# Kernel optimization log

Measured on AMD Instinct MI355X. Metric: run time of the kernel, lower is better.

## Reference

```python
import jax, jax.numpy as jnp
import numpy as np

NUM_HEADS = 16
ROPE_BASE = 10000.0


def apply_rope(x):
    # x: [B, T, H, D]; torchtune-style interleaved-pair RoPE, positions 0..T-1
    B, T, H, D = x.shape
    inv_freq = 1.0 / (ROPE_BASE ** (jnp.arange(0, D, 2, dtype=jnp.float32) / D))  # [D/2]
    pos = jnp.arange(T, dtype=jnp.float32)
    freqs = pos[:, None] * inv_freq[None, :]              # [T, D/2]
    cos = jnp.cos(freqs)[None, :, None, :].astype(x.dtype)
    sin = jnp.sin(freqs)[None, :, None, :].astype(x.dtype)
    x1 = x[..., 0::2]
    x2 = x[..., 1::2]
    o1 = x1 * cos - x2 * sin
    o2 = x2 * cos + x1 * sin
    return jnp.stack([o1, o2], axis=-1).reshape(B, T, H, D)


def setup_inputs() -> dict:
    key = jax.random.key(0)
    k1, k2, k3 = jax.random.split(key, 3)
    B, T, C = 2, 8192, 1024
    x = jax.random.normal(k1, (B, T, C), dtype=jnp.float32)
    # torch Linear weight layout [out_features, in_features]; fan-in scaling
    Wqkv = jax.random.normal(k2, (3 * C, C), dtype=jnp.float32) * (C ** -0.5)
    Wout = jax.random.normal(k3, (C, C), dtype=jnp.float32) * (C ** -0.5)
    return {"x": x, "Wqkv": Wqkv, "Wout": Wout}


def reference(x, Wqkv, Wout):
    B, T, C = x.shape
    H = NUM_HEADS
    D = C // H
    qkv = (x @ Wqkv.T).reshape(B, T, 3, H, D)
    q, k, v = qkv[:, :, 0], qkv[:, :, 1], qkv[:, :, 2]   # each [B, T, H, D]
    q = apply_rope(q)
    k = apply_rope(k)
    # Faithful to source: SDPA is called on [B, T, H, D] WITHOUT transposing,
    # so torch attends over the heads axis (L = H) with (B, T) as batch dims.
    scale = 1.0 / jnp.sqrt(jnp.asarray(D, dtype=x.dtype))
    scores = jnp.einsum('btqd,btkd->btqk', q, k) * scale  # [B, T, H, H]
    attn = jax.nn.softmax(scores, axis=-1)
    out = jnp.einsum('btqk,btkd->btqd', attn, v)          # [B, T, H, D]
    # Replicate attn_output.transpose(1, 2).contiguous().view(B, T, C)
    out = out.transpose(0, 2, 1, 3).reshape(B, T, C)
    return out @ Wout.T
```

## Files before the change

### kernel.cpp

```cpp
#include <hip/hip_runtime.h>
#include <stdint.h>

#define TT 8192
#define BT 16384
#define MCH 8192

typedef __attribute__((ext_vector_type(8))) __bf16 bf16x8;
typedef __attribute__((ext_vector_type(4))) __bf16 bf16x4;
typedef __attribute__((ext_vector_type(4))) short short4v;
typedef __attribute__((ext_vector_type(4))) float floatx4;

__device__ __forceinline__ float bf2f(unsigned short h) {
  union { unsigned u; float f; } x; x.u = ((unsigned)h) << 16; return x.f;
}
__device__ __forceinline__ unsigned short f2bf(float f) {
  union { float f; unsigned u; } x; x.f = f;
  unsigned r = (x.u + 0x7fffu + ((x.u >> 16) & 1u)) >> 16;
  return (unsigned short)r;
}
__device__ __forceinline__ void async16(const void* g, void* l) {
  __builtin_amdgcn_global_load_lds(
      (__attribute__((address_space(1))) void*)g,
      (__attribute__((address_space(3))) void*)l, 16, 0, 0);
}

__global__ __launch_bounds__(256) void cvt_f2b(
    const float* __restrict__ src, unsigned short* __restrict__ dst, int n4) {
  const int i = blockIdx.x * 256 + threadIdx.x;
  if (i < n4) {
    const float4 f = ((const float4*)src)[i];
    union { uint2 u2; unsigned short s[4]; } o;
    o.s[0] = f2bf(f.x); o.s[1] = f2bf(f.y);
    o.s[2] = f2bf(f.z); o.s[3] = f2bf(f.w);
    ((uint2*)dst)[i] = o.u2;
  }
}

__global__ __launch_bounds__(256) void prep_k(
    const float* __restrict__ Wqkv, const float* __restrict__ Wout,
    unsigned short* __restrict__ Wqkvb, unsigned short* __restrict__ Woutb,
    float2* __restrict__ tab) {
  const int bx = blockIdx.x;
  const int tid = threadIdx.x;
  if (bx < 1024) {
    const int i = bx * 256 + tid;
    const int t = i >> 5, p = i & 31;
    const float f = (float)t * exp2f((float)p * -0.41524101186092f);
    float s, c;
    sincosf(f, &s, &c);
    tab[i] = make_float2(c, s);
  } else {
    const float* src;
    unsigned short* dst;
    int i;
    if (bx < 4096) { src = Wqkv; dst = Wqkvb; i = (bx - 1024) * 256 + tid; }
    else           { src = Wout; dst = Woutb; i = (bx - 4096) * 256 + tid; }
    const float4 f = ((const float4*)src)[i];
    union { uint2 u2; unsigned short s[4]; } o;
    o.s[0] = f2bf(f.x); o.s[1] = f2bf(f.y);
    o.s[2] = f2bf(f.z); o.s[3] = f2bf(f.w);
    ((uint2*)dst)[i] = o.u2;
  }
}

template <bool CF32>
__global__ __launch_bounds__(512, 4) void gemm_k32(
    const unsigned short* __restrict__ A,
    const unsigned short* __restrict__ W,
    void* __restrict__ C,
    int M, int N, int K)
{
  __shared__ __align__(16) unsigned short sm[2][(256 + 128) * 32];

  const int tid  = threadIdx.x;
  const int lane = tid & 63;
  const int wid  = tid >> 6;
  const int wr   = wid >> 1;
  const int wc   = wid & 1;
  const int lm   = lane & 15;
  const int kg   = lane >> 4;
  const int cxor = (lm >> 1) & 3;

  const int nb  = N >> 7;
  const int cpx = (int)gridDim.x >> 3;
  const int bid = blockIdx.x;
  const int swz = (bid & 7) * cpx + (bid >> 3);
  const int bm  = swz / nb;
  const int bn  = swz % nb;

  const int NT = K >> 5;

  const int sr  = lane >> 2;
  const int scb = lane & 3;
  const unsigned short* gsrc0;
  const unsigned short* gsrc1;
  const unsigned short* gsrc2;
  {
    const int r0 = wid * 16 + sr;
    const int r1 = 128 + r0;
    const int rB = wid * 16 + sr;
    gsrc0 = A + (size_t)(bm * 256 + r0) * (size_t)K + ((scb ^ ((r0 >> 1) & 3)) << 3);
    gsrc1 = A + (size_t)(bm * 256 + r1) * (size_t)K + ((scb ^ ((r1 >> 1) & 3)) << 3);
    gsrc2 = W + (size_t)(bn * 128 + rB) * (size_t)K + ((scb ^ ((rB >> 1) & 3)) << 3);
  }
  const int ld0 = wid * 1024;
  const int ld1 = 8192 + wid * 1024;
  const int ld2 = 16384 + wid * 1024;

  auto stage_tile = [&](int tt) {
    char* lb = (char*)sm[tt & 1];
    const size_t koff = (size_t)tt << 5;
    async16(gsrc0 + koff, lb + ld0);
    async16(gsrc1 + koff, lb + ld1);
    async16(gsrc2 + koff, lb + ld2);
  };

  floatx4 acc[4][4];
  floatx4 z = {0.f, 0.f, 0.f, 0.f};
#pragma unroll
  for (int i = 0; i < 4; ++i)
#pragma unroll
    for (int j = 0; j < 4; ++j) acc[i][j] = z;

  stage_tile(0);
  stage_tile(1);
  asm volatile("s_waitcnt vmcnt(3)" ::: "memory");
  __builtin_amdgcn_s_barrier();
  __builtin_amdgcn_sched_barrier(0);

  for (int t = 0; t < NT; ++t) {
    const unsigned short* Ab = sm[t & 1];
    const unsigned short* Bb = Ab + 256 * 32;

    bf16x8 af[4], bfr[4];
#pragma unroll
    for (int i = 0; i < 4; ++i) {
      const int rr = wr * 64 + i * 16 + lm;
      af[i] = *(const bf16x8*)(Ab + rr * 32 + ((kg ^ cxor) << 3));
    }
#pragma unroll
    for (int j = 0; j < 4; ++j) {
      const int rr = wc * 64 + j * 16 + lm;
      bfr[j] = *(const bf16x8*)(Bb + rr * 32 + ((kg ^ cxor) << 3));
    }

    __builtin_amdgcn_s_barrier();
    asm volatile("s_waitcnt lgkmcnt(0)" ::: "memory");
    __builtin_amdgcn_sched_barrier(0);

    if (t + 2 < NT) stage_tile(t + 2);

    __builtin_amdgcn_s_setprio(1);
#pragma unroll
    for (int i = 0; i < 4; ++i)
#pragma unroll
      for (int j = 0; j < 4; ++j)
        acc[i][j] = __builtin_amdgcn_mfma_f32_16x16x32_bf16(
            af[i], bfr[j], acc[i][j], 0, 0, 0);
    __builtin_amdgcn_s_setprio(0);

    if (t + 1 < NT) {
      if (t + 2 < NT)
        asm volatile("s_waitcnt vmcnt(3)" ::: "memory");
      else
        asm volatile("s_waitcnt vmcnt(0)" ::: "memory");
      __builtin_amdgcn_s_barrier();
      __builtin_amdgcn_sched_barrier(0);
    }
  }

#pragma unroll
  for (int i = 0; i < 4; ++i) {
    const int row0 = bm * 256 + wr * 64 + i * 16 + kg * 4;
#pragma unroll
    for (int j = 0; j < 4; ++j) {
      const int col = bn * 128 + wc * 64 + j * 16 + lm;
#pragma unroll
      for (int r = 0; r < 4; ++r) {
        if (CF32)
          ((float*)C)[(size_t)(row0 + r) * N + col] = acc[i][j][r];
        else
          ((unsigned short*)C)[(size_t)(row0 + r) * N + col] = f2bf(acc[i][j][r]);
      }
    }
  }
}

#if defined(__has_builtin)
#if __has_builtin(__builtin_amdgcn_mfma_f32_16x16x16_bf16)
#define PV_MFMA 1
#define PV_MFMA_CALL(a, b, c) __builtin_amdgcn_mfma_f32_16x16x16_bf16( \
    *(bf16x4*)&(a), *(bf16x4*)&(b), (c), 0, 0, 0)
#elif __has_builtin(__builtin_amdgcn_mfma_f32_16x16x16bf16_1k)
#define PV_MFMA 1
#define PV_MFMA_CALL(a, b, c) __builtin_amdgcn_mfma_f32_16x16x16bf16_1k( \
    (a), (b), (c), 0, 0, 0)
#else
#define PV_MFMA 0
#endif
#else
#define PV_MFMA 0
#endif

__global__ __launch_bounds__(256, 4) void attn_rope_k(
    const unsigned short* __restrict__ qkv,
    const float2* __restrict__ tab,
    unsigned short* __restrict__ Y,
    int base)
{
  __shared__ __align__(16) unsigned short sV[4][16 * 72];
#if !PV_MFMA
  __shared__ float sP[4][256];
#endif

  const int wave = threadIdx.x >> 6;
  const int lane = threadIdx.x & 63;
  const int lm   = lane & 15;
  const int quad = lane >> 4;
  const int ml0  = blockIdx.x * 8 + wave * 2;
  unsigned short* VB = sV[wave];

  const int hlo = lane >> 3;
  const int d0  = (lane & 7) * 8;
  const int p0  = d0 >> 1;

  uint4 R[2][6];
  float4 CS[2][2];
  int tA[2], bA[2];
#pragma unroll
  for (int tk = 0; tk < 2; ++tk) {
    const int m = base + ml0 + tk;
    tA[tk] = m & (TT - 1);
    bA[tk] = m >> 13;
    const uint4* row = (const uint4*)(qkv + (size_t)(ml0 + tk) * 3072);
#pragma unroll
    for (int i = 0; i < 6; ++i) R[tk][i] = row[lane + 64 * i];
    CS[tk][0] = *(const float4*)(tab + (tA[tk] << 5) + p0);
    CS[tk][1] = *(const float4*)(tab + (tA[tk] << 5) + p0 + 2);
  }

#pragma unroll
  for (int tk = 0; tk < 2; ++tk) {
    const int t = tA[tk];
    const float cs[4] = {CS[tk][0].x, CS[tk][0].z, CS[tk][1].x, CS[tk][1].z};
    const float sn[4] = {CS[tk][0].y, CS[tk][0].w, CS[tk][1].y, CS[tk][1].w};

    uint4 P[4];
#pragma unroll
    for (int i = 0; i < 4; ++i) {
      union { uint4 u4; unsigned short s[8]; } cv;
      cv.u4 = R[tk][i];
      float f[8];
#pragma unroll
      for (int j = 0; j < 8; ++j) f[j] = bf2f(cv.s[j]);
#pragma unroll
      for (int j = 0; j < 4; ++j) {
        const float x1 = f[2 * j], x2 = f[2 * j + 1];
        cv.s[2 * j]     = f2bf(x1 * cs[j] - x2 * sn[j]);
        cv.s[2 * j + 1] = f2bf(x2 * cs[j] + x1 * sn[j]);
      }
      P[i] = cv.u4;
    }

    *(uint4*)(VB + hlo * 72 + d0)       = R[tk][4];
    *(uint4*)(VB + (8 + hlo) * 72 + d0) = R[tk][5];

    __builtin_amdgcn_s_setprio(1);
    floatx4 accS = {0.f, 0.f, 0.f, 0.f};
#pragma unroll
    for (int half = 0; half < 2; ++half) {
      const int bpi = (((lm & 7) * 8) + half * 4 + quad) * 4;
      union { int w[4]; bf16x8 v; } kf, qf;
#pragma unroll
      for (int w = 0; w < 4; ++w) {
        const int q0 = __builtin_amdgcn_ds_bpermute(bpi, (int)(&P[0].x)[w]);
        const int q1 = __builtin_amdgcn_ds_bpermute(bpi, (int)(&P[1].x)[w]);
        qf.w[w] = lm < 8 ? q0 : q1;
        const int k0 = __builtin_amdgcn_ds_bpermute(bpi, (int)(&P[2].x)[w]);
        const int k1 = __builtin_amdgcn_ds_bpermute(bpi, (int)(&P[3].x)[w]);
        kf.w[w] = lm < 8 ? k0 : k1;
      }
      accS = __builtin_amdgcn_mfma_f32_16x16x32_bf16(kf.v, qf.v, accS, 0, 0, 0);
    }

    float s4[4];
    float mx = -1e30f;
#pragma unroll
    for (int j = 0; j < 4; ++j) { s4[j] = accS[j] * 0.125f; mx = fmaxf(mx, s4[j]); }
    mx = fmaxf(mx, __shfl_xor(mx, 16, 64));
    mx = fmaxf(mx, __shfl_xor(mx, 32, 64));
    float sum = 0.f;
#pragma unroll
    for (int j = 0; j < 4; ++j) { s4[j] = __expf(s4[j] - mx); sum += s4[j]; }
    sum += __shfl_xor(sum, 16, 64);
    sum += __shfl_xor(sum, 32, 64);
    const float inv = 1.0f / sum;

#if PV_MFMA
    union { short4v v; unsigned short s[4]; } pf;
#pragma unroll
    for (int j = 0; j < 4; ++j) pf.s[j] = f2bf(s4[j] * inv);
    unsigned short vs[16];
#pragma unroll
    for (int dtile = 0; dtile < 4; ++dtile)
#pragma unroll
      for (int j = 0; j < 4; ++j)
        vs[dtile * 4 + j] = VB[(quad * 4 + j) * 72 + dtile * 16 + lm];
#pragma unroll
    for (int dtile = 0; dtile < 4; ++dtile) {
      union { short4v v; unsigned short s[4]; } vf;
#pragma unroll
      for (int j = 0; j < 4; ++j) vf.s[j] = vs[dtile * 4 + j];
      floatx4 accO = {0.f, 0.f, 0.f, 0.f};
      accO = PV_MFMA_CALL(pf.v, vf.v, accO);
      const int col = (t & 15) * 64 + dtile * 16 + lm;
#pragma unroll
      for (int r = 0; r < 4; ++r) {
        const size_t rr = (size_t)bA[tk] * TT + (size_t)(quad * 4 + r) * 512 + (t >> 4);
        Y[rr * 1024 + col] = f2bf(accO[r]);
      }
    }
    __builtin_amdgcn_s_setprio(0);
#else
    __builtin_amdgcn_s_setprio(0);
    float* Pp = sP[wave];
#pragma unroll
    for (int j = 0; j < 4; ++j) Pp[(quad * 4 + j) * 16 + lm] = s4[j] * inv;
    asm volatile("s_waitcnt lgkmcnt(0)" ::: "memory");
    __builtin_amdgcn_sched_barrier(0);
    float o[16];
#pragma unroll
    for (int dd = 0; dd < 16; ++dd) o[dd] = 0.f;
#pragma unroll
    for (int kh = 0; kh < 16; ++kh) {
      const float a = Pp[kh * 16 + lm];
      union { uint4 u4; unsigned short s[8]; } v0, v1;
      v0.u4 = *(const uint4*)(VB + kh * 72 + quad * 16);
      v1.u4 = *(const uint4*)(VB + kh * 72 + quad * 16 + 8);
#pragma unroll
      for (int dd = 0; dd < 8; ++dd) {
        o[dd]     += a * bf2f(v0.s[dd]);
        o[dd + 8] += a * bf2f(v1.s[dd]);
      }
    }
    const size_t rr = (size_t)bA[tk] * TT + (size_t)lm * 512 + (t >> 4);
    unsigned short* yp = Y + rr * 1024 + (t & 15) * 64 + quad * 16;
    union { uint4 u4; unsigned short s[8]; } o1, o2;
#pragma unroll
    for (int dd = 0; dd < 8; ++dd) o1.s[dd] = f2bf(o[dd]);
#pragma unroll
    for (int dd = 0; dd < 8; ++dd) o2.s[dd] = f2bf(o[8 + dd]);
    ((uint4*)yp)[0] = o1.u4;
    ((uint4*)yp)[1] = o2.u4;
#endif
  }
}

extern "C" void kernel_launch(void* const* d_in, const int* in_sizes, int n_in,
                              void* d_out, int out_size, void* d_ws, size_t ws_size,
                              hipStream_t stream) {
  const float* x    = (const float*)d_in[0];
  const float* Wqkv = (const float*)d_in[1];
  const float* Wout = (const float*)d_in[2];
  float* out = (float*)d_out;

  unsigned short* Y     = (unsigned short*)d_ws;
  unsigned short* Wqkvb = Y + (size_t)BT * 1024;
  unsigned short* Woutb = Wqkvb + (size_t)3072 * 1024;
  unsigned short* xb    = Woutb + (size_t)1024 * 1024;
  unsigned short* qkvC  = (unsigned short*)d_out;
  float2* tab           = (float2*)((char*)d_out + (size_t)52 * 1024 * 1024);

  prep_k<<<dim3(5120), dim3(256), 0, stream>>>(Wqkv, Wout, Wqkvb, Woutb, tab);

  for (int base = 0; base < BT; base += MCH) {
    cvt_f2b<<<dim3(MCH * 1024 / 4 / 256), dim3(256), 0, stream>>>(
        x + (size_t)base * 1024, xb, MCH * 1024 / 4);
    gemm_k32<false><<<dim3((MCH / 256) * (3072 / 128)), dim3(512), 0, stream>>>(
        xb, Wqkvb, qkvC, MCH, 3072, 1024);
    attn_rope_k<<<dim3(MCH / 8), dim3(256), 0, stream>>>(qkvC, tab, Y, base);
  }

  gemm_k32<true><<<dim3((BT / 256) * (1024 / 128)), dim3(512), 0, stream>>>(
      Y, Woutb, out, BT, 1024, 1024);
}
```

Baseline: 312.5 us.

## Stage attention output in LDS for coalesced 16-byte stores, one token per wave

```diff
diff --git a/kernel.cpp b/kernel.cpp
--- a/kernel.cpp
+++ b/kernel.cpp
@@ -209,6 +209,7 @@
     int base)
 {
   __shared__ __align__(16) unsigned short sV[4][16 * 72];
+  __shared__ __align__(16) unsigned short sO[4][1024];
 #if !PV_MFMA
   __shared__ float sP[4][256];
 #endif
@@ -217,142 +218,139 @@
   const int lane = threadIdx.x & 63;
   const int lm   = lane & 15;
   const int quad = lane >> 4;
-  const int ml0  = blockIdx.x * 8 + wave * 2;
+  const int ml   = blockIdx.x * 4 + wave;
+  const int m    = base + ml;
+  const int t    = m & (TT - 1);
   unsigned short* VB = sV[wave];
 
   const int hlo = lane >> 3;
   const int d0  = (lane & 7) * 8;
   const int p0  = d0 >> 1;
 
-  uint4 R[2][6];
-  float4 CS[2][2];
-  int tA[2], bA[2];
-#pragma unroll
-  for (int tk = 0; tk < 2; ++tk) {
-    const int m = base + ml0 + tk;
-    tA[tk] = m & (TT - 1);
-    bA[tk] = m >> 13;
-    const uint4* row = (const uint4*)(qkv + (size_t)(ml0 + tk) * 3072);
-#pragma unroll
-    for (int i = 0; i < 6; ++i) R[tk][i] = row[lane + 64 * i];
-    CS[tk][0] = *(const float4*)(tab + (tA[tk] << 5) + p0);
-    CS[tk][1] = *(const float4*)(tab + (tA[tk] << 5) + p0 + 2);
-  }
-
-#pragma unroll
-  for (int tk = 0; tk < 2; ++tk) {
-    const int t = tA[tk];
-    const float cs[4] = {CS[tk][0].x, CS[tk][0].z, CS[tk][1].x, CS[tk][1].z};
-    const float sn[4] = {CS[tk][0].y, CS[tk][0].w, CS[tk][1].y, CS[tk][1].w};
-
-    uint4 P[4];
-#pragma unroll
-    for (int i = 0; i < 4; ++i) {
-      union { uint4 u4; unsigned short s[8]; } cv;
-      cv.u4 = R[tk][i];
-      float f[8];
-#pragma unroll
-      for (int j = 0; j < 8; ++j) f[j] = bf2f(cv.s[j]);
-#pragma unroll
-      for (int j = 0; j < 4; ++j) {
-        const float x1 = f[2 * j], x2 = f[2 * j + 1];
-        cv.s[2 * j]     = f2bf(x1 * cs[j] - x2 * sn[j]);
-        cv.s[2 * j + 1] = f2bf(x2 * cs[j] + x1 * sn[j]);
-      }
-      P[i] = cv.u4;
-    }
-
-    *(uint4*)(VB + hlo * 72 + d0)       = R[tk][4];
-    *(uint4*)(VB + (8 + hlo) * 72 + d0) = R[tk][5];
-
-    __builtin_amdgcn_s_setprio(1);
-    floatx4 accS = {0.f, 0.f, 0.f, 0.f};
-#pragma unroll
-    for (int half = 0; half < 2; ++half) {
-      const int bpi = (((lm & 7) * 8) + half * 4 + quad) * 4;
-      union { int w[4]; bf16x8 v; } kf, qf;
-#pragma unroll
-      for (int w = 0; w < 4; ++w) {
-        const int q0 = __builtin_amdgcn_ds_bpermute(bpi, (int)(&P[0].x)[w]);
-        const int q1 = __builtin_amdgcn_ds_bpermute(bpi, (int)(&P[1].x)[w]);
-        qf.w[w] = lm < 8 ? q0 : q1;
-        const int k0 = __builtin_amdgcn_ds_bpermute(bpi, (int)(&P[2].x)[w]);
-        const int k1 = __builtin_amdgcn_ds_bpermute(bpi, (int)(&P[3].x)[w]);
-        kf.w[w] = lm < 8 ? k0 : k1;
-      }
-      accS = __builtin_amdgcn_mfma_f32_16x16x32_bf16(kf.v, qf.v, accS, 0, 0, 0);
-    }
-
-    float s4[4];
-    float mx = -1e30f;
-#pragma unroll
-    for (int j = 0; j < 4; ++j) { s4[j] = accS[j] * 0.125f; mx = fmaxf(mx, s4[j]); }
-    mx = fmaxf(mx, __shfl_xor(mx, 16, 64));
-    mx = fmaxf(mx, __shfl_xor(mx, 32, 64));
-    float sum = 0.f;
-#pragma unroll
-    for (int j = 0; j < 4; ++j) { s4[j] = __expf(s4[j] - mx); sum += s4[j]; }
-    sum += __shfl_xor(sum, 16, 64);
-    sum += __shfl_xor(sum, 32, 64);
-    const float inv = 1.0f / sum;
+  uint4 R[6];
+  const uint4* row = (const uint4*)(qkv + (size_t)ml * 3072);
+#pragma unroll
+  for (int i = 0; i < 6; ++i) R[i] = row[lane + 64 * i];
+  const float4 CS0 = *(const float4*)(tab + (t << 5) + p0);
+  const float4 CS1 = *(const float4*)(tab + (t << 5) + p0 + 2);
+  const float cs[4] = {CS0.x, CS0.z, CS1.x, CS1.z};
+  const float sn[4] = {CS0.y, CS0.w, CS1.y, CS1.w};
+
+  uint4 P[4];
+#pragma unroll
+  for (int i = 0; i < 4; ++i) {
+    union { uint4 u4; unsigned short s[8]; } cv;
+    cv.u4 = R[i];
+    float f[8];
+#pragma unroll
+    for (int j = 0; j < 8; ++j) f[j] = bf2f(cv.s[j]);
+#pragma unroll
+    for (int j = 0; j < 4; ++j) {
+      const float x1 = f[2 * j], x2 = f[2 * j + 1];
+      cv.s[2 * j]     = f2bf(x1 * cs[j] - x2 * sn[j]);
+      cv.s[2 * j + 1] = f2bf(x2 * cs[j] + x1 * sn[j]);
+    }
+    P[i] = cv.u4;
+  }
+
+  *(uint4*)(VB + hlo * 72 + d0)       = R[4];
+  *(uint4*)(VB + (8 + hlo) * 72 + d0) = R[5];
+
+  __builtin_amdgcn_s_setprio(1);
+  floatx4 accS = {0.f, 0.f, 0.f, 0.f};
+#pragma unroll
+  for (int half = 0; half < 2; ++half) {
+    const int bpi = (((lm & 7) * 8) + half * 4 + quad) * 4;
+    union { int w[4]; bf16x8 v; } kf, qf;
+#pragma unroll
+    for (int w = 0; w < 4; ++w) {
+      const int q0 = __builtin_amdgcn_ds_bpermute(bpi, (int)(&P[0].x)[w]);
+      const int q1 = __builtin_amdgcn_ds_bpermute(bpi, (int)(&P[1].x)[w]);
+      qf.w[w] = lm < 8 ? q0 : q1;
+      const int k0 = __builtin_amdgcn_ds_bpermute(bpi, (int)(&P[2].x)[w]);
+      const int k1 = __builtin_amdgcn_ds_bpermute(bpi, (int)(&P[3].x)[w]);
+      kf.w[w] = lm < 8 ? k0 : k1;
+    }
+    accS = __builtin_amdgcn_mfma_f32_16x16x32_bf16(kf.v, qf.v, accS, 0, 0, 0);
+  }
+
+  float s4[4];
+  float mx = -1e30f;
+#pragma unroll
+  for (int j = 0; j < 4; ++j) { s4[j] = accS[j] * 0.125f; mx = fmaxf(mx, s4[j]); }
+  mx = fmaxf(mx, __shfl_xor(mx, 16, 64));
+  mx = fmaxf(mx, __shfl_xor(mx, 32, 64));
+  float sum = 0.f;
+#pragma unroll
+  for (int j = 0; j < 4; ++j) { s4[j] = __expf(s4[j] - mx); sum += s4[j]; }
+  sum += __shfl_xor(sum, 16, 64);
+  sum += __shfl_xor(sum, 32, 64);
+  const float inv = 1.0f / sum;
 
 #if PV_MFMA
-    union { short4v v; unsigned short s[4]; } pf;
-#pragma unroll
-    for (int j = 0; j < 4; ++j) pf.s[j] = f2bf(s4[j] * inv);
-    unsigned short vs[16];
-#pragma unroll
-    for (int dtile = 0; dtile < 4; ++dtile)
-#pragma unroll
-      for (int j = 0; j < 4; ++j)
-        vs[dtile * 4 + j] = VB[(quad * 4 + j) * 72 + dtile * 16 + lm];
-#pragma unroll
-    for (int dtile = 0; dtile < 4; ++dtile) {
-      union { short4v v; unsigned short s[4]; } vf;
-#pragma unroll
-      for (int j = 0; j < 4; ++j) vf.s[j] = vs[dtile * 4 + j];
-      floatx4 accO = {0.f, 0.f, 0.f, 0.f};
-      accO = PV_MFMA_CALL(pf.v, vf.v, accO);
-      const int col = (t & 15) * 64 + dtile * 16 + lm;
-#pragma unroll
-      for (int r = 0; r < 4; ++r) {
-        const size_t rr = (size_t)bA[tk] * TT + (size_t)(quad * 4 + r) * 512 + (t >> 4);
-        Y[rr * 1024 + col] = f2bf(accO[r]);
-      }
-    }
-    __builtin_amdgcn_s_setprio(0);
+  union { short4v v; unsigned short s[4]; } pf;
+#pragma unroll
+  for (int j = 0; j < 4; ++j) pf.s[j] = f2bf(s4[j] * inv);
+  unsigned short vs[16];
+#pragma unroll
+  for (int dtile = 0; dtile < 4; ++dtile)
+#pragma unroll
+    for (int j = 0; j < 4; ++j)
+      vs[dtile * 4 + j] = VB[(quad * 4 + j) * 72 + dtile * 16 + lm];
+#pragma unroll
+  for (int dtile = 0; dtile < 4; ++dtile) {
+    union { short4v v; unsigned short s[4]; } vf;
+#pragma unroll
+    for (int j = 0; j < 4; ++j) vf.s[j] = vs[dtile * 4 + j];
+    floatx4 accO = {0.f, 0.f, 0.f, 0.f};
+    accO = PV_MFMA_CALL(pf.v, vf.v, accO);
+#pragma unroll
+    for (int r = 0; r < 4; ++r)
+      sO[wave][(quad * 4 + r) * 64 + dtile * 16 + lm] = f2bf(accO[r]);
+  }
+  __builtin_amdgcn_s_setprio(0);
 #else
-    __builtin_amdgcn_s_setprio(0);
-    float* Pp = sP[wave];
-#pragma unroll
-    for (int j = 0; j < 4; ++j) Pp[(quad * 4 + j) * 16 + lm] = s4[j] * inv;
-    asm volatile("s_waitcnt lgkmcnt(0)" ::: "memory");
-    __builtin_amdgcn_sched_barrier(0);
-    float o[16];
-#pragma unroll
-    for (int dd = 0; dd < 16; ++dd) o[dd] = 0.f;
-#pragma unroll
-    for (int kh = 0; kh < 16; ++kh) {
-      const float a = Pp[kh * 16 + lm];
-      union { uint4 u4; unsigned short s[8]; } v0, v1;
-      v0.u4 = *(const uint4*)(VB + kh * 72 + quad * 16);
-      v1.u4 = *(const uint4*)(VB + kh * 72 + quad * 16 + 8);
-#pragma unroll
-      for (int dd = 0; dd < 8; ++dd) {
-        o[dd]     += a * bf2f(v0.s[dd]);
-        o[dd + 8] += a * bf2f(v1.s[dd]);
-      }
-    }
-    const size_t rr = (size_t)bA[tk] * TT + (size_t)lm * 512 + (t >> 4);
-    unsigned short* yp = Y + rr * 1024 + (t & 15) * 64 + quad * 16;
-    union { uint4 u4; unsigned short s[8]; } o1, o2;
-#pragma unroll
-    for (int dd = 0; dd < 8; ++dd) o1.s[dd] = f2bf(o[dd]);
-#pragma unroll
-    for (int dd = 0; dd < 8; ++dd) o2.s[dd] = f2bf(o[8 + dd]);
-    ((uint4*)yp)[0] = o1.u4;
-    ((uint4*)yp)[1] = o2.u4;
+  __builtin_amdgcn_s_setprio(0);
+  float* Pp = sP[wave];
+#pragma unroll
+  for (int j = 0; j < 4; ++j) Pp[(quad * 4 + j) * 16 + lm] = s4[j] * inv;
+  asm volatile("s_waitcnt lgkmcnt(0)" ::: "memory");
+  __builtin_amdgcn_sched_barrier(0);
+  float o[16];
+#pragma unroll
+  for (int dd = 0; dd < 16; ++dd) o[dd] = 0.f;
+#pragma unroll
+  for (int kh = 0; kh < 16; ++kh) {
+    const float a = Pp[kh * 16 + lm];
+    union { uint4 u4; unsigned short s[8]; } v0, v1;
+    v0.u4 = *(const uint4*)(VB + kh * 72 + quad * 16);
+    v1.u4 = *(const uint4*)(VB + kh * 72 + quad * 16 + 8);
+#pragma unroll
+    for (int dd = 0; dd < 8; ++dd) {
+      o[dd]     += a * bf2f(v0.s[dd]);
+      o[dd + 8] += a * bf2f(v1.s[dd]);
+    }
+  }
+#pragma unroll
+  for (int dd = 0; dd < 16; ++dd)
+    sO[wave][lm * 64 + quad * 16 + dd] = f2bf(o[dd]);
 #endif
+
+  __syncthreads();
+  const int m0 = base + blockIdx.x * 4;
+  const int t0 = m0 & (TT - 1);
+  const int b0 = m0 >> 13;
+#pragma unroll
+  for (int s = 0; s < 2; ++s) {
+    const int u   = threadIdx.x + s * 256;
+    const int qh  = u >> 5;
+    const int rem = u & 31;
+    const int tk  = rem >> 3;
+    const int e8  = (rem & 7) * 8;
+    const uint4 v = *(const uint4*)(&sO[tk][qh * 64 + e8]);
+    const size_t off = (((size_t)(b0 * TT + qh * 512 + (t0 >> 4))) << 10)
+                       + (t0 & 15) * 64 + rem * 8;
+    *(uint4*)(Y + off) = v;
   }
 }
 
@@ -378,7 +376,7 @@
         x + (size_t)base * 1024, xb, MCH * 1024 / 4);
     gemm_k32<false><<<dim3((MCH / 256) * (3072 / 128)), dim3(512), 0, stream>>>(
         xb, Wqkvb, qkvC, MCH, 3072, 1024);
-    attn_rope_k<<<dim3(MCH / 8), dim3(256), 0, stream>>>(qkvC, tab, Y, base);
+    attn_rope_k<<<dim3(MCH / 4), dim3(256), 0, stream>>>(qkvC, tab, Y, base);
   }
 
   gemm_k32<true><<<dim3((BT / 256) * (1024 / 128)), dim3(512), 0, stream>>>(
```

Measured after the change: 312.0 us. Within noise of the previous version (-0.2%).
